# Performance work log

Hardware: AMD Instinct MI355X
Metric: run time of the kernel (lower is better)

The kernel has to match this reference:

```python
import jax, jax.numpy as jnp
import numpy as np

B, C, H, W = 8, 128, 48, 48
GROUPS = 32
EPS = 1e-5


def group_norm(x, w, b):
    # x: [B,C,H,W] -> normalize within 32 groups over (C//G, H, W)
    xg = x.reshape(B, GROUPS, C // GROUPS, H, W)
    mu = xg.mean(axis=(2, 3, 4), keepdims=True)
    var = xg.var(axis=(2, 3, 4), keepdims=True)
    xg = (xg - mu) * jax.lax.rsqrt(var + EPS)
    return xg.reshape(B, C, H, W) * w[None, :, None, None] + b[None, :, None, None]


def conv1x1(x, w, b):
    # pointwise conv: [B,C,H,W], w: [Cout,Cin], b: [Cout]
    return jnp.einsum('oc,bchw->bohw', w, x) + b[None, :, None, None]


def setup_inputs() -> dict:
    key = jax.random.key(0)
    ks = jax.random.split(key, 6)
    s = 1.0 / np.sqrt(C)
    return {
        'x': jax.random.normal(ks[0], (B, C, H, W), jnp.float32),
        'gn_w': jnp.ones((C,), jnp.float32),
        'gn_b': jnp.zeros((C,), jnp.float32),
        'wq': jax.random.normal(ks[1], (C, C), jnp.float32) * s,
        'bq': jnp.zeros((C,), jnp.float32),
        'wk': jax.random.normal(ks[2], (C, C), jnp.float32) * s,
        'bk': jnp.zeros((C,), jnp.float32),
        'wv': jax.random.normal(ks[3], (C, C), jnp.float32) * s,
        'bv': jnp.zeros((C,), jnp.float32),
        'wo': jax.random.normal(ks[4], (C, C), jnp.float32) * s,
        'bo': jnp.zeros((C,), jnp.float32),
    }


def reference(x, gn_w, gn_b, wq, bq, wk, bk, wv, bv, wo, bo):
    xn = group_norm(x, gn_w, gn_b)
    q = conv1x1(xn, wq, bq)
    k = conv1x1(xn, wk, bk)
    v = conv1x1(xn, wv, bv)
    # scores: [B,H,W,I,J]
    scores = jnp.einsum('bchw,bcij->bhwij', q, k) / jnp.sqrt(jnp.float32(C))
    # NOTE: original calls F.softmax with no dim; torch picks dim=1 (the query-H axis)
    attn = jax.nn.softmax(scores, axis=1)
    ctx = jnp.einsum('bhwnm,bcnm->bchw', attn, v)
    return x + conv1x1(ctx, wo, bo)
```

## Files before the change

kernel.cpp:

```cpp
#include <hip/hip_runtime.h>
#include <hip/hip_bf16.h>

typedef short s16x8 __attribute__((ext_vector_type(8)));
typedef float f32x4 __attribute__((ext_vector_type(4)));
typedef int   i32x4 __attribute__((ext_vector_type(4)));
typedef unsigned short u16;

#define BB 8
#define CC 128
#define HH 48
#define WW 48
#define NN 2304
#define SCALE_L2E 0.12751744f
#define SZ_MAP (BB*CC*NN)
#define NSPLIT 3
#define TILES_PER (18/NSPLIT)

__device__ inline u16 f2bf(float f) {
    unsigned u = __builtin_bit_cast(unsigned, f);
    u = (u + 0x7FFFu + ((u >> 16) & 1u)) >> 16;
    return (u16)u;
}
__device__ inline float bf2f(u16 h) {
    unsigned u = ((unsigned)h) << 16;
    return __builtin_bit_cast(float, u);
}

#define MFMA(a, b, c) __builtin_amdgcn_mfma_f32_16x16x32_bf16(a, b, c, 0, 0, 0)
#define DPP_ROR_ADD(x, N) { \
    int yi_ = __builtin_amdgcn_update_dpp(0, __builtin_bit_cast(int, x), 0x120 | (N), 0xf, 0xf, true); \
    x += __builtin_bit_cast(float, yi_); }

__global__ __launch_bounds__(256) void gnprep_kernel(
        const float* __restrict__ x, const float* __restrict__ gw,
        const float* __restrict__ gb, u16* __restrict__ xnT,
        const float* __restrict__ wq, const float* __restrict__ wk,
        const float* __restrict__ wv_, const float* __restrict__ wo,
        u16* __restrict__ w16) {
    int tid = threadIdx.x;
    if (blockIdx.x >= 256) {
        int i = (blockIdx.x - 256) * 256 + tid;
        int m = i >> 14, r = i & 16383;
        const float* src = (m == 0) ? wq : (m == 1) ? wk : (m == 2) ? wv_ : wo;
        w16[i] = f2bf(src[r]);
        return;
    }
    int b = blockIdx.x & 7, g = blockIdx.x >> 3;
    const float* xb = x + ((size_t)b * CC + g * 4) * NN;
    float v[4][9];
    float s = 0.f, ss = 0.f;
#pragma unroll
    for (int c = 0; c < 4; ++c)
#pragma unroll
        for (int k = 0; k < 9; ++k) {
            float t = xb[c * NN + tid + k * 256];
            v[c][k] = t; s += t; ss += t * t;
        }
#pragma unroll
    for (int o = 32; o > 0; o >>= 1) { s += __shfl_down(s, o); ss += __shfl_down(ss, o); }
    __shared__ float red[8];
    __shared__ float stats[2];
    int wid = tid >> 6;
    if ((tid & 63) == 0) { red[wid * 2] = s; red[wid * 2 + 1] = ss; }
    __syncthreads();
    if (tid == 0) {
        float S = 0.f, SS = 0.f;
        for (int i = 0; i < 4; ++i) { S += red[i * 2]; SS += red[i * 2 + 1]; }
        float mu = S * (1.f / 9216.f);
        float var = SS * (1.f / 9216.f) - mu * mu;
        stats[0] = mu;
        stats[1] = rsqrtf(var + 1e-5f);
    }
    __syncthreads();
    float mu = stats[0], rs = stats[1];
    float sc[4], bi[4];
#pragma unroll
    for (int c = 0; c < 4; ++c) {
        sc[c] = gw[g * 4 + c] * rs;
        bi[c] = gb[g * 4 + c] - mu * sc[c];
    }
#pragma unroll
    for (int k = 0; k < 9; ++k) {
        int n = tid + k * 256;
        ushort4 o;
        o.x = f2bf(v[0][k] * sc[0] + bi[0]);
        o.y = f2bf(v[1][k] * sc[1] + bi[1]);
        o.z = f2bf(v[2][k] * sc[2] + bi[2]);
        o.w = f2bf(v[3][k] * sc[3] + bi[3]);
        *(ushort4*)(xnT + ((size_t)b * NN + n) * CC + g * 4) = o;
    }
}

__global__ __launch_bounds__(256) void qkv_kernel(
        const u16* __restrict__ xnT, const u16* __restrict__ w16,
        const float* __restrict__ bq, const float* __restrict__ bk,
        const float* __restrict__ bv,
        u16* __restrict__ qT, u16* __restrict__ kt2, u16* __restrict__ vt2) {
    int b = blockIdx.x, n0 = blockIdx.y * 128, z = blockIdx.z;
    int tid = threadIdx.x, lane = tid & 63, wvw = tid >> 6;
    int l15 = lane & 15, l4 = lane >> 4;
    const u16* xb = xnT + (size_t)b * NN * CC;

    if (z == 0) {
        const u16* w16q = w16;
        const u16* w16k = w16 + 16384;
        u16* kb = kt2 + (size_t)b * NN * CC;
        s16x8 xa[2][4];
#pragma unroll
        for (int mf = 0; mf < 2; ++mf)
#pragma unroll
            for (int ks = 0; ks < 4; ++ks)
                xa[mf][ks] = *(const s16x8*)(xb + (size_t)(n0 + wvw * 32 + mf * 16 + l15) * CC + ks * 32 + l4 * 8);
#pragma unroll 2
        for (int nf = 0; nf < 8; ++nf) {
            f32x4 aq[2] = {}, ak[2] = {};
#pragma unroll
            for (int ks = 0; ks < 4; ++ks) {
                s16x8 fq = *(const s16x8*)(w16q + (nf * 16 + l15) * CC + ks * 32 + l4 * 8);
                s16x8 fk = *(const s16x8*)(w16k + (nf * 16 + l15) * CC + ks * 32 + l4 * 8);
#pragma unroll
                for (int mf = 0; mf < 2; ++mf) {
                    aq[mf] = MFMA(xa[mf][ks], fq, aq[mf]);
                    ak[mf] = MFMA(xa[mf][ks], fk, ak[mf]);
                }
            }
            int co = nf * 16 + l15;
            float bql = bq[co], bkl = bk[co];
            int chunk = blockIdx.y * 4 + wvw;
#pragma unroll
            for (int mf = 0; mf < 2; ++mf)
#pragma unroll
                for (int r = 0; r < 4; ++r) {
                    int n = n0 + wvw * 32 + mf * 16 + l4 * 4 + r;
                    qT[((size_t)b * NN + n) * CC + co] = f2bf((aq[mf][r] + bql) * SCALE_L2E);
                    int slot = (l4 & 1) * 16 + mf * 8 + (l4 >> 1) * 4 + r;
                    kb[(size_t)chunk * 4096 + (co >> 5) * 1024 + slot * 32 + (co & 31)]
                        = f2bf(ak[mf][r] + bkl);
                }
        }
    } else {
        const u16* w16v = w16 + 2 * 16384;
        u16* vb = vt2 + (size_t)b * NN * CC;
        s16x8 wa[2][4];
#pragma unroll
        for (int mf = 0; mf < 2; ++mf)
#pragma unroll
            for (int ks = 0; ks < 4; ++ks)
                wa[mf][ks] = *(const s16x8*)(w16v + (wvw * 32 + mf * 16 + l15) * CC + ks * 32 + l4 * 8);
#pragma unroll 2
        for (int nf = 0; nf < 8; ++nf) {
            f32x4 av[2] = {};
#pragma unroll
            for (int ks = 0; ks < 4; ++ks) {
                s16x8 xf = *(const s16x8*)(xb + (size_t)(n0 + nf * 16 + l15) * CC + ks * 32 + l4 * 8);
#pragma unroll
                for (int mf = 0; mf < 2; ++mf) av[mf] = MFMA(wa[mf][ks], xf, av[mf]);
            }
            int chunk = blockIdx.y * 4 + (nf >> 1);
            int n_off = (nf & 1) * 16 + l15;
#pragma unroll
            for (int mf = 0; mf < 2; ++mf) {
                int co = wvw * 32 + mf * 16 + l4 * 4;
#pragma unroll
                for (int r = 0; r < 4; ++r) {
                    int c = co + r;
                    float bvl = bv[c];
                    vb[(size_t)chunk * 4096 + (c >> 4) * 512 + (c & 15) * 32 + n_off]
                        = f2bf(av[mf][r] + bvl);
                }
            }
        }
    }
}

#define TILE_BODY(T, KFC, KFN) { \
    const u16* cv = vb + (size_t)((T) * 4 + wvw) * 4096; \
    s16x8 vf[8]; \
    _Pragma("unroll") \
    for (int cf = 0; cf < 8; ++cf) \
        vf[cf] = *(const s16x8*)(cv + cf * 512 + l15 * 32 + l4 * 8); \
    f32x4 sf[2][3] = {}; \
    __builtin_amdgcn_s_setprio(1); \
    _Pragma("unroll") \
    for (int ks = 0; ks < 4; ++ks) \
        _Pragma("unroll") \
        for (int mf = 0; mf < 2; ++mf) \
            _Pragma("unroll") \
            for (int hf = 0; hf < 3; ++hf) \
                sf[mf][hf] = MFMA(KFC[mf][ks], qf[hf][ks], sf[mf][hf]); \
    __builtin_amdgcn_s_setprio(0); \
    { \
        int tn_ = ((T) + 1 < 18) ? (T) + 1 : 0; \
        const u16* cbn_ = kb + (size_t)(tn_ * 4 + wvw) * 4096; \
        _Pragma("unroll") \
        for (int mf = 0; mf < 2; ++mf) \
            _Pragma("unroll") \
            for (int ks = 0; ks < 4; ++ks) \
                KFN[mf][ks] = *(const s16x8*)(cbn_ + ks * 1024 + (mf * 16 + l15) * 32 + l4 * 8); \
    } \
    float p[2][3][4]; \
    _Pragma("unroll") \
    for (int mf = 0; mf < 2; ++mf) \
        _Pragma("unroll") \
        for (int hf = 0; hf < 3; ++hf) \
            _Pragma("unroll") \
            for (int r = 0; r < 4; ++r) p[mf][hf][r] = __builtin_amdgcn_exp2f(sf[mf][hf][r]); \
    float den[2][4]; \
    _Pragma("unroll") \
    for (int mf = 0; mf < 2; ++mf) \
        _Pragma("unroll") \
        for (int r = 0; r < 4; ++r) \
            den[mf][r] = p[mf][0][r] + p[mf][1][r] + p[mf][2][r]; \
    _Pragma("unroll") \
    for (int mf = 0; mf < 2; ++mf) \
        _Pragma("unroll") \
        for (int r = 0; r < 4; ++r) { \
            DPP_ROR_ADD(den[mf][r], 1); \
            DPP_ROR_ADD(den[mf][r], 2); \
            DPP_ROR_ADD(den[mf][r], 4); \
            DPP_ROR_ADD(den[mf][r], 8); \
        } \
    float rd[2][4]; \
    _Pragma("unroll") \
    for (int mf = 0; mf < 2; ++mf) \
        _Pragma("unroll") \
        for (int r = 0; r < 4; ++r) rd[mf][r] = __builtin_amdgcn_rcpf(den[mf][r]); \
    s16x8 pbf[3]; \
    _Pragma("unroll") \
    for (int hf = 0; hf < 3; ++hf) { \
        unsigned u0, u1, u2, u3; \
        float a0 = p[0][hf][0] * rd[0][0], a1 = p[0][hf][1] * rd[0][1]; \
        float a2 = p[0][hf][2] * rd[0][2], a3 = p[0][hf][3] * rd[0][3]; \
        float a4 = p[1][hf][0] * rd[1][0], a5 = p[1][hf][1] * rd[1][1]; \
        float a6 = p[1][hf][2] * rd[1][2], a7 = p[1][hf][3] * rd[1][3]; \
        asm("v_cvt_pk_bf16_f32 %0, %1, %2" : "=v"(u0) : "v"(a0), "v"(a1)); \
        asm("v_cvt_pk_bf16_f32 %0, %1, %2" : "=v"(u1) : "v"(a2), "v"(a3)); \
        asm("v_cvt_pk_bf16_f32 %0, %1, %2" : "=v"(u2) : "v"(a4), "v"(a5)); \
        asm("v_cvt_pk_bf16_f32 %0, %1, %2" : "=v"(u3) : "v"(a6), "v"(a7)); \
        i32x4 bb2 = { (int)u0, (int)u1, (int)u2, (int)u3 }; \
        pbf[hf] = __builtin_bit_cast(s16x8, bb2); \
    } \
    __builtin_amdgcn_s_setprio(1); \
    _Pragma("unroll") \
    for (int cf = 0; cf < 8; ++cf) \
        _Pragma("unroll") \
        for (int hf = 0; hf < 3; ++hf) \
            cacc[cf][hf] = MFMA(vf[cf], pbf[hf], cacc[cf][hf]); \
    __builtin_amdgcn_s_setprio(0); \
}

__global__ __launch_bounds__(256, 2) void attn_kernel(
        const u16* __restrict__ qT, const u16* __restrict__ kt2,
        const u16* __restrict__ vt2, u16* __restrict__ part) {
    int b = blockIdx.x, w = blockIdx.y, sp = blockIdx.z;
    int tid = threadIdx.x, lane = tid & 63, wvw = tid >> 6;
    int l15 = lane & 15, l4 = lane >> 4;
    __shared__ float red[4 * 48 * 36];

    const u16* qb = qT + (size_t)b * NN * CC;
    const u16* kb = kt2 + (size_t)b * NN * CC;
    const u16* vb = vt2 + (size_t)b * NN * CC;

    s16x8 qf[3][4];
#pragma unroll
    for (int hf = 0; hf < 3; ++hf)
#pragma unroll
        for (int ks = 0; ks < 4; ++ks)
            qf[hf][ks] = *(const s16x8*)(qb + (size_t)((hf * 16 + l15) * WW + w) * CC + ks * 32 + l4 * 8);

    f32x4 cacc[8][3] = {};

    const int tbase = sp * TILES_PER;

    s16x8 kfA[2][4], kfB[2][4];
    {
        const u16* cb = kb + (size_t)(tbase * 4 + wvw) * 4096;
#pragma unroll
        for (int mf = 0; mf < 2; ++mf)
#pragma unroll
            for (int ks = 0; ks < 4; ++ks)
                kfA[mf][ks] = *(const s16x8*)(cb + ks * 1024 + (mf * 16 + l15) * 32 + l4 * 8);
    }

#pragma unroll 1
    for (int tt = 0; tt < TILES_PER; tt += 2) {
        int t0 = tbase + tt;
        TILE_BODY(t0, kfA, kfB)
        int t1 = tbase + tt + 1;
        TILE_BODY(t1, kfB, kfA)
    }

#pragma unroll
    for (int s = 0; s < 4; ++s) {
        if (s) __syncthreads();
#pragma unroll
        for (int q = 0; q < 4; ++q) {
            if (((q - wvw) & 3) == s) {
#pragma unroll
                for (int i = 0; i < 2; ++i) {
                    int cf = 2 * q + i;
#pragma unroll
                    for (int hf = 0; hf < 3; ++hf) {
                        int addr = q * 1728 + (hf * 16 + l15) * 36 + i * 16 + 4 * l4;
                        f32x4* pp = (f32x4*)&red[addr];
                        if (s == 0) *pp = cacc[cf][hf];
                        else { f32x4 tv = *pp; tv += cacc[cf][hf]; *pp = tv; }
                    }
                }
            }
        }
    }
    __syncthreads();
    u16* po = part + (size_t)(b * NSPLIT + sp) * NN * CC;
#pragma unroll
    for (int pass = 0; pass < 12; ++pass) {
        int h = pass * 4 + l4;
        int c = wvw * 32 + l15 * 2;
        float2 v2 = *(float2*)&red[wvw * 1728 + h * 36 + l15 * 2];
        unsigned pk;
        asm("v_cvt_pk_bf16_f32 %0, %1, %2" : "=v"(pk) : "v"(v2.x), "v"(v2.y));
        *(unsigned*)(po + (size_t)(h * WW + w) * CC + c) = pk;
    }
}

__global__ __launch_bounds__(256) void out_kernel(
        const u16* __restrict__ part, const u16* __restrict__ w16o,
        const float* __restrict__ bo, const float* __restrict__ x,
        float* __restrict__ out) {
    int b = blockIdx.x, n0 = blockIdx.y * 128;
    int tid = threadIdx.x, lane = tid & 63, wvw = tid >> 6;
    int l15 = lane & 15, l4 = lane >> 4;
    const u16* pb = part + (size_t)b * NSPLIT * NN * CC;
    s16x8 bfr[2][4];
#pragma unroll
    for (int nf = 0; nf < 2; ++nf)
#pragma unroll
        for (int ks = 0; ks < 4; ++ks) {
            size_t off = (size_t)(n0 + wvw * 32 + nf * 16 + l15) * CC + ks * 32 + l4 * 8;
            s16x8 v0 = *(const s16x8*)(pb + off);
            s16x8 v1 = *(const s16x8*)(pb + (size_t)NN * CC + off);
            s16x8 v2 = *(const s16x8*)(pb + (size_t)2 * NN * CC + off);
            s16x8 o;
#pragma unroll
            for (int j = 0; j < 8; ++j)
                o[j] = (short)f2bf(bf2f((u16)v0[j]) + bf2f((u16)v1[j]) + bf2f((u16)v2[j]));
            bfr[nf][ks] = o;
        }
#pragma unroll 2
    for (int mf = 0; mf < 8; ++mf) {
        s16x8 af[4];
#pragma unroll
        for (int ks = 0; ks < 4; ++ks)
            af[ks] = *(const s16x8*)(w16o + (mf * 16 + l15) * CC + ks * 32 + l4 * 8);
        f32x4 acc[2] = {};
#pragma unroll
        for (int ks = 0; ks < 4; ++ks)
#pragma unroll
            for (int nf = 0; nf < 2; ++nf)
                acc[nf] = MFMA(af[ks], bfr[nf][ks], acc[nf]);
#pragma unroll
        for (int nf = 0; nf < 2; ++nf)
#pragma unroll
            for (int r = 0; r < 4; ++r) {
                int co = mf * 16 + l4 * 4 + r;
                int n = n0 + wvw * 32 + nf * 16 + l15;
                size_t idx = ((size_t)b * CC + co) * NN + n;
                out[idx] = acc[nf][r] + bo[co] + x[idx];
            }
    }
}

extern "C" void kernel_launch(void* const* d_in, const int* in_sizes, int n_in,
                              void* d_out, int out_size, void* d_ws, size_t ws_size,
                              hipStream_t stream) {
    const float* x  = (const float*)d_in[0];
    const float* gw = (const float*)d_in[1];
    const float* gb = (const float*)d_in[2];
    const float* wq = (const float*)d_in[3];
    const float* bq = (const float*)d_in[4];
    const float* wk = (const float*)d_in[5];
    const float* bk = (const float*)d_in[6];
    const float* wv_ = (const float*)d_in[7];
    const float* bv = (const float*)d_in[8];
    const float* wo = (const float*)d_in[9];
    const float* bo = (const float*)d_in[10];

    u16* ws   = (u16*)d_ws;
    u16* xnT  = ws;
    u16* qT   = ws + (size_t)SZ_MAP;
    u16* kt2  = ws + (size_t)2 * SZ_MAP;
    u16* vt2  = ws + (size_t)3 * SZ_MAP;
    u16* part = ws + (size_t)4 * SZ_MAP;
    u16* w16  = ws + (size_t)(4 + NSPLIT) * SZ_MAP;
    float* out = (float*)d_out;

    gnprep_kernel<<<512, 256, 0, stream>>>(x, gw, gb, xnT, wq, wk, wv_, wo, w16);
    qkv_kernel<<<dim3(8, 18, 2), 256, 0, stream>>>(xnT, w16, bq, bk, bv, qT, kt2, vt2);
    attn_kernel<<<dim3(8, WW, NSPLIT), 256, 0, stream>>>(qT, kt2, vt2, part);
    out_kernel<<<dim3(8, 18), 256, 0, stream>>>(part, w16 + 3 * 16384, bo, x, out);
}
```

Measured before the change: 86.86 us.

## Assign one query column per wave instead of splitting keys across waves

Each wave in the attention kernel now owns its own query column w and walks all of its key chunks, rather than the four waves sharing one column and splitting the key chunks between them. This drops the LDS cross-wave reduction and its barriers, and each wave writes its accumulators straight to the partial buffer. The block count falls by a factor of four, and each wave loops over 24 chunks instead of 6. The four waves in a block now read the same K/V chunks, which could improve cache reuse, while the added per-iteration __syncthreads keeps the waves in lockstep.

```diff
diff --git a/kernel.cpp b/kernel.cpp
--- a/kernel.cpp
+++ b/kernel.cpp
@@ -14,7 +14,7 @@
 #define SCALE_L2E 0.12751744f
 #define SZ_MAP (BB*CC*NN)
 #define NSPLIT 3
-#define TILES_PER (18/NSPLIT)
+#define CHPER 24
 
 __device__ inline u16 f2bf(float f) {
     unsigned u = __builtin_bit_cast(unsigned, f);
@@ -173,8 +173,8 @@
     }
 }
 
-#define TILE_BODY(T, KFC, KFN) { \
-    const u16* cv = vb + (size_t)((T) * 4 + wvw) * 4096; \
+#define TILE_BODY(CH, KFC, KFN) { \
+    const u16* cv = vb + (size_t)(CH) * 4096; \
     s16x8 vf[8]; \
     _Pragma("unroll") \
     for (int cf = 0; cf < 8; ++cf) \
@@ -190,8 +190,8 @@
                 sf[mf][hf] = MFMA(KFC[mf][ks], qf[hf][ks], sf[mf][hf]); \
     __builtin_amdgcn_s_setprio(0); \
     { \
-        int tn_ = ((T) + 1 < 18) ? (T) + 1 : 0; \
-        const u16* cbn_ = kb + (size_t)(tn_ * 4 + wvw) * 4096; \
+        int cn_ = ((CH) + 1 < 72) ? (CH) + 1 : 0; \
+        const u16* cbn_ = kb + (size_t)cn_ * 4096; \
         _Pragma("unroll") \
         for (int mf = 0; mf < 2; ++mf) \
             _Pragma("unroll") \
@@ -252,10 +252,10 @@
 __global__ __launch_bounds__(256, 2) void attn_kernel(
         const u16* __restrict__ qT, const u16* __restrict__ kt2,
         const u16* __restrict__ vt2, u16* __restrict__ part) {
-    int b = blockIdx.x, w = blockIdx.y, sp = blockIdx.z;
+    int b = blockIdx.x, sp = blockIdx.z;
     int tid = threadIdx.x, lane = tid & 63, wvw = tid >> 6;
+    int w = blockIdx.y * 4 + wvw;
     int l15 = lane & 15, l4 = lane >> 4;
-    __shared__ float red[4 * 48 * 36];
 
     const u16* qb = qT + (size_t)b * NN * CC;
     const u16* kb = kt2 + (size_t)b * NN * CC;
@@ -270,11 +270,11 @@
 
     f32x4 cacc[8][3] = {};
 
-    const int tbase = sp * TILES_PER;
+    const int cbase = sp * CHPER;
 
     s16x8 kfA[2][4], kfB[2][4];
     {
-        const u16* cb = kb + (size_t)(tbase * 4 + wvw) * 4096;
+        const u16* cb = kb + (size_t)cbase * 4096;
 #pragma unroll
         for (int mf = 0; mf < 2; ++mf)
 #pragma unroll
@@ -283,44 +283,27 @@
     }
 
 #pragma unroll 1
-    for (int tt = 0; tt < TILES_PER; tt += 2) {
-        int t0 = tbase + tt;
-        TILE_BODY(t0, kfA, kfB)
-        int t1 = tbase + tt + 1;
-        TILE_BODY(t1, kfB, kfA)
-    }
-
-#pragma unroll
-    for (int s = 0; s < 4; ++s) {
-        if (s) __syncthreads();
-#pragma unroll
-        for (int q = 0; q < 4; ++q) {
-            if (((q - wvw) & 3) == s) {
-#pragma unroll
-                for (int i = 0; i < 2; ++i) {
-                    int cf = 2 * q + i;
-#pragma unroll
-                    for (int hf = 0; hf < 3; ++hf) {
-                        int addr = q * 1728 + (hf * 16 + l15) * 36 + i * 16 + 4 * l4;
-                        f32x4* pp = (f32x4*)&red[addr];
-                        if (s == 0) *pp = cacc[cf][hf];
-                        else { f32x4 tv = *pp; tv += cacc[cf][hf]; *pp = tv; }
-                    }
-                }
-            }
-        }
-    }
-    __syncthreads();
+    for (int ii = 0; ii < CHPER; ii += 2) {
+        int c0 = cbase + ii;
+        TILE_BODY(c0, kfA, kfB)
+        int c1 = cbase + ii + 1;
+        TILE_BODY(c1, kfB, kfA)
+        __syncthreads();
+    }
+
     u16* po = part + (size_t)(b * NSPLIT + sp) * NN * CC;
 #pragma unroll
-    for (int pass = 0; pass < 12; ++pass) {
-        int h = pass * 4 + l4;
-        int c = wvw * 32 + l15 * 2;
-        float2 v2 = *(float2*)&red[wvw * 1728 + h * 36 + l15 * 2];
-        unsigned pk;
-        asm("v_cvt_pk_bf16_f32 %0, %1, %2" : "=v"(pk) : "v"(v2.x), "v"(v2.y));
-        *(unsigned*)(po + (size_t)(h * WW + w) * CC + c) = pk;
-    }
+    for (int cf = 0; cf < 8; ++cf)
+#pragma unroll
+        for (int hf = 0; hf < 3; ++hf) {
+            int h = hf * 16 + l15;
+            int c0 = cf * 16 + l4 * 4;
+            unsigned pk01, pk23;
+            asm("v_cvt_pk_bf16_f32 %0, %1, %2" : "=v"(pk01) : "v"(cacc[cf][hf][0]), "v"(cacc[cf][hf][1]));
+            asm("v_cvt_pk_bf16_f32 %0, %1, %2" : "=v"(pk23) : "v"(cacc[cf][hf][2]), "v"(cacc[cf][hf][3]));
+            uint2 pk = { pk01, pk23 };
+            *(uint2*)(po + (size_t)(h * WW + w) * CC + c0) = pk;
+        }
 }
 
 __global__ __launch_bounds__(256) void out_kernel(
@@ -396,6 +379,6 @@
 
     gnprep_kernel<<<512, 256, 0, stream>>>(x, gw, gb, xnT, wq, wk, wv_, wo, w16);
     qkv_kernel<<<dim3(8, 18, 2), 256, 0, stream>>>(xnT, w16, bq, bk, bv, qT, kt2, vt2);
-    attn_kernel<<<dim3(8, WW, NSPLIT), 256, 0, stream>>>(qT, kt2, vt2, part);
+    attn_kernel<<<dim3(8, 12, NSPLIT), 256, 0, stream>>>(qT, kt2, vt2, part);
     out_kernel<<<dim3(8, 18), 256, 0, stream>>>(part, w16 + 3 * 16384, bo, x, out);
 }
```

Result: slower. 100.7 us (+15.9%).

## Software-pipeline QK scores one tile ahead of softmax and PV

Applied to the files above, without the earlier changes.

Restructures the attention tile loop so the QK MFMAs for the next tile are issued right after the exponentials of the current tile. The K fragments are now prefetched two tiles ahead, and the V loads are moved later. A prologue computes the first tile's scores and a drain macro finishes the last tile. The aim is to overlap MFMA work with the transcendental, DPP reduction and load latency, at the cost of extra accumulator registers, which could cause spills or lower occupancy under launch_bounds(256,2).

```diff
diff --git a/kernel.cpp b/kernel.cpp
--- a/kernel.cpp
+++ b/kernel.cpp
@@ -173,13 +173,19 @@
     }
 }
 
-#define TILE_BODY(T, KFC, KFN) { \
-    const u16* cv = vb + (size_t)((T) * 4 + wvw) * 4096; \
-    s16x8 vf[8]; \
-    _Pragma("unroll") \
-    for (int cf = 0; cf < 8; ++cf) \
-        vf[cf] = *(const s16x8*)(cv + cf * 512 + l15 * 32 + l4 * 8); \
-    f32x4 sf[2][3] = {}; \
+#define FULL(T, SFP, SFQ, KFN, KFP) { \
+    float p[2][3][4]; \
+    _Pragma("unroll") \
+    for (int mf = 0; mf < 2; ++mf) \
+        _Pragma("unroll") \
+        for (int hf = 0; hf < 3; ++hf) \
+            _Pragma("unroll") \
+            for (int r = 0; r < 4; ++r) p[mf][hf][r] = __builtin_amdgcn_exp2f(SFP[mf][hf][r]); \
+    _Pragma("unroll") \
+    for (int mf = 0; mf < 2; ++mf) \
+        _Pragma("unroll") \
+        for (int hf = 0; hf < 3; ++hf) \
+            SFQ[mf][hf] = (f32x4){0.f, 0.f, 0.f, 0.f}; \
     __builtin_amdgcn_s_setprio(1); \
     _Pragma("unroll") \
     for (int ks = 0; ks < 4; ++ks) \
@@ -187,30 +193,19 @@
         for (int mf = 0; mf < 2; ++mf) \
             _Pragma("unroll") \
             for (int hf = 0; hf < 3; ++hf) \
-                sf[mf][hf] = MFMA(KFC[mf][ks], qf[hf][ks], sf[mf][hf]); \
+                SFQ[mf][hf] = MFMA(KFN[mf][ks], qf[hf][ks], SFQ[mf][hf]); \
     __builtin_amdgcn_s_setprio(0); \
-    { \
-        int tn_ = ((T) + 1 < 18) ? (T) + 1 : 0; \
-        const u16* cbn_ = kb + (size_t)(tn_ * 4 + wvw) * 4096; \
-        _Pragma("unroll") \
-        for (int mf = 0; mf < 2; ++mf) \
-            _Pragma("unroll") \
-            for (int ks = 0; ks < 4; ++ks) \
-                KFN[mf][ks] = *(const s16x8*)(cbn_ + ks * 1024 + (mf * 16 + l15) * 32 + l4 * 8); \
-    } \
-    float p[2][3][4]; \
-    _Pragma("unroll") \
-    for (int mf = 0; mf < 2; ++mf) \
-        _Pragma("unroll") \
-        for (int hf = 0; hf < 3; ++hf) \
-            _Pragma("unroll") \
-            for (int r = 0; r < 4; ++r) p[mf][hf][r] = __builtin_amdgcn_exp2f(sf[mf][hf][r]); \
     float den[2][4]; \
     _Pragma("unroll") \
     for (int mf = 0; mf < 2; ++mf) \
         _Pragma("unroll") \
         for (int r = 0; r < 4; ++r) \
             den[mf][r] = p[mf][0][r] + p[mf][1][r] + p[mf][2][r]; \
+    const u16* cv = vb + (size_t)((T) * 4 + wvw) * 4096; \
+    s16x8 vf[8]; \
+    _Pragma("unroll") \
+    for (int cf = 0; cf < 8; ++cf) \
+        vf[cf] = *(const s16x8*)(cv + cf * 512 + l15 * 32 + l4 * 8); \
     _Pragma("unroll") \
     for (int mf = 0; mf < 2; ++mf) \
         _Pragma("unroll") \
@@ -220,6 +215,15 @@
             DPP_ROR_ADD(den[mf][r], 4); \
             DPP_ROR_ADD(den[mf][r], 8); \
         } \
+    { \
+        int tn_ = ((T) + 2 < 18) ? (T) + 2 : 0; \
+        const u16* cbn_ = kb + (size_t)(tn_ * 4 + wvw) * 4096; \
+        _Pragma("unroll") \
+        for (int mf = 0; mf < 2; ++mf) \
+            _Pragma("unroll") \
+            for (int ks = 0; ks < 4; ++ks) \
+                KFP[mf][ks] = *(const s16x8*)(cbn_ + ks * 1024 + (mf * 16 + l15) * 32 + l4 * 8); \
+    } \
     float rd[2][4]; \
     _Pragma("unroll") \
     for (int mf = 0; mf < 2; ++mf) \
@@ -249,6 +253,63 @@
     __builtin_amdgcn_s_setprio(0); \
 }
 
+#define DRAIN(T, SFP) { \
+    float p[2][3][4]; \
+    _Pragma("unroll") \
+    for (int mf = 0; mf < 2; ++mf) \
+        _Pragma("unroll") \
+        for (int hf = 0; hf < 3; ++hf) \
+            _Pragma("unroll") \
+            for (int r = 0; r < 4; ++r) p[mf][hf][r] = __builtin_amdgcn_exp2f(SFP[mf][hf][r]); \
+    float den[2][4]; \
+    _Pragma("unroll") \
+    for (int mf = 0; mf < 2; ++mf) \
+        _Pragma("unroll") \
+        for (int r = 0; r < 4; ++r) \
+            den[mf][r] = p[mf][0][r] + p[mf][1][r] + p[mf][2][r]; \
+    const u16* cv = vb + (size_t)((T) * 4 + wvw) * 4096; \
+    s16x8 vf[8]; \
+    _Pragma("unroll") \
+    for (int cf = 0; cf < 8; ++cf) \
+        vf[cf] = *(const s16x8*)(cv + cf * 512 + l15 * 32 + l4 * 8); \
+    _Pragma("unroll") \
+    for (int mf = 0; mf < 2; ++mf) \
+        _Pragma("unroll") \
+        for (int r = 0; r < 4; ++r) { \
+            DPP_ROR_ADD(den[mf][r], 1); \
+            DPP_ROR_ADD(den[mf][r], 2); \
+            DPP_ROR_ADD(den[mf][r], 4); \
+            DPP_ROR_ADD(den[mf][r], 8); \
+        } \
+    float rd[2][4]; \
+    _Pragma("unroll") \
+    for (int mf = 0; mf < 2; ++mf) \
+        _Pragma("unroll") \
+        for (int r = 0; r < 4; ++r) rd[mf][r] = __builtin_amdgcn_rcpf(den[mf][r]); \
+    s16x8 pbf[3]; \
+    _Pragma("unroll") \
+    for (int hf = 0; hf < 3; ++hf) { \
+        unsigned u0, u1, u2, u3; \
+        float a0 = p[0][hf][0] * rd[0][0], a1 = p[0][hf][1] * rd[0][1]; \
+        float a2 = p[0][hf][2] * rd[0][2], a3 = p[0][hf][3] * rd[0][3]; \
+        float a4 = p[1][hf][0] * rd[1][0], a5 = p[1][hf][1] * rd[1][1]; \
+        float a6 = p[1][hf][2] * rd[1][2], a7 = p[1][hf][3] * rd[1][3]; \
+        asm("v_cvt_pk_bf16_f32 %0, %1, %2" : "=v"(u0) : "v"(a0), "v"(a1)); \
+        asm("v_cvt_pk_bf16_f32 %0, %1, %2" : "=v"(u1) : "v"(a2), "v"(a3)); \
+        asm("v_cvt_pk_bf16_f32 %0, %1, %2" : "=v"(u2) : "v"(a4), "v"(a5)); \
+        asm("v_cvt_pk_bf16_f32 %0, %1, %2" : "=v"(u3) : "v"(a6), "v"(a7)); \
+        i32x4 bb2 = { (int)u0, (int)u1, (int)u2, (int)u3 }; \
+        pbf[hf] = __builtin_bit_cast(s16x8, bb2); \
+    } \
+    __builtin_amdgcn_s_setprio(1); \
+    _Pragma("unroll") \
+    for (int cf = 0; cf < 8; ++cf) \
+        _Pragma("unroll") \
+        for (int hf = 0; hf < 3; ++hf) \
+            cacc[cf][hf] = MFMA(vf[cf], pbf[hf], cacc[cf][hf]); \
+    __builtin_amdgcn_s_setprio(0); \
+}
+
 __global__ __launch_bounds__(256, 2) void attn_kernel(
         const u16* __restrict__ qT, const u16* __restrict__ kt2,
         const u16* __restrict__ vt2, u16* __restrict__ part) {
@@ -273,6 +334,7 @@
     const int tbase = sp * TILES_PER;
 
     s16x8 kfA[2][4], kfB[2][4];
+    f32x4 sfA[2][3], sfB[2][3];
     {
         const u16* cb = kb + (size_t)(tbase * 4 + wvw) * 4096;
 #pragma unroll
@@ -281,13 +343,39 @@
             for (int ks = 0; ks < 4; ++ks)
                 kfA[mf][ks] = *(const s16x8*)(cb + ks * 1024 + (mf * 16 + l15) * 32 + l4 * 8);
     }
+#pragma unroll
+    for (int mf = 0; mf < 2; ++mf)
+#pragma unroll
+        for (int hf = 0; hf < 3; ++hf)
+            sfA[mf][hf] = (f32x4){0.f, 0.f, 0.f, 0.f};
+#pragma unroll
+    for (int ks = 0; ks < 4; ++ks)
+#pragma unroll
+        for (int mf = 0; mf < 2; ++mf)
+#pragma unroll
+            for (int hf = 0; hf < 3; ++hf)
+                sfA[mf][hf] = MFMA(kfA[mf][ks], qf[hf][ks], sfA[mf][hf]);
+    {
+        const u16* cb = kb + (size_t)((tbase + 1) * 4 + wvw) * 4096;
+#pragma unroll
+        for (int mf = 0; mf < 2; ++mf)
+#pragma unroll
+            for (int ks = 0; ks < 4; ++ks)
+                kfB[mf][ks] = *(const s16x8*)(cb + ks * 1024 + (mf * 16 + l15) * 32 + l4 * 8);
+    }
 
 #pragma unroll 1
-    for (int tt = 0; tt < TILES_PER; tt += 2) {
+    for (int tt = 0; tt < TILES_PER - 2; tt += 2) {
         int t0 = tbase + tt;
-        TILE_BODY(t0, kfA, kfB)
+        FULL(t0, sfA, sfB, kfB, kfA)
         int t1 = tbase + tt + 1;
-        TILE_BODY(t1, kfB, kfA)
+        FULL(t1, sfB, sfA, kfA, kfB)
+    }
+    {
+        int t4 = tbase + TILES_PER - 2;
+        FULL(t4, sfA, sfB, kfB, kfA)
+        int t5 = tbase + TILES_PER - 1;
+        DRAIN(t5, sfB)
     }
 
 #pragma unroll
```

New measurement: 136.3 us. 1.57x slower.
